# Optimization experiments

Measured on AMD Instinct MI355X. Metric: run time of the kernel, lower is better.

The kernel has to match this reference:

```python
import jax, jax.numpy as jnp
import numpy as np

B, D_IN, N, L, P, C = 512, 784, 2048, 6, 15, 10  # batch, input, width, dag layers, weight pairs, classes


def setup_inputs() -> dict:
    key = jax.random.key(0)
    ks = jax.random.split(key, 10)
    x = jax.random.normal(ks[0], (B, D_IN), jnp.float32)
    w_in = jax.random.normal(ks[1], (N, D_IN), jnp.float32) * 0.1
    b_in = jax.random.normal(ks[2], (N,), jnp.float32) * 0.1
    W = jax.random.normal(ks[3], (P, N, N), jnp.float32) * 0.1
    # binary 0/1 float masks standing in for DAG connectivity masks
    M = jax.random.bernoulli(ks[4], 0.5, (P, N, N)).astype(jnp.float32)
    b = jax.random.normal(ks[5], (L - 1, N), jnp.float32) * 0.1
    w_out1 = jax.random.normal(ks[6], (C, N), jnp.float32) * 0.1
    b_out1 = jax.random.normal(ks[7], (C,), jnp.float32) * 0.1
    w_out2 = jax.random.normal(ks[8], (C, N), jnp.float32) * 0.1
    b_out2 = jax.random.normal(ks[9], (C,), jnp.float32) * 0.1
    return {"x": x, "w_in": w_in, "b_in": b_in, "W": W, "M": M, "b": b,
            "w_out1": w_out1, "b_out1": b_out1, "w_out2": w_out2, "b_out2": b_out2}


def reference(x, w_in, b_in, W, M, b, w_out1, b_out1, w_out2, b_out2):
    # input layer
    acts = [jax.nn.relu(x @ w_in.T + b_in)]  # [B, N]
    idx = 0
    for i in range(1, L):  # DAG layer i has predecessors 0..i-1
        Wm = W[idx:idx + i] * M[idx:idx + i]          # [i, N, N] masked weights
        stacked = jnp.stack(acts)                      # [i, B, N]
        # sum over predecessors of inp @ Wm.T; bias added once per predecessor
        out = jnp.einsum('jbn,jmn->bm', stacked, Wm) + i * b[i - 1]
        acts.append(jax.nn.relu(out))
        idx += i
    return acts[-1] @ w_out1.T + b_out1 + acts[-2] @ w_out2.T + b_out2
```

## Files before the change

### kernel.cpp

```cpp
#include <hip/hip_runtime.h>

typedef __bf16 bf16;
typedef __attribute__((ext_vector_type(8))) __bf16 bf16x8;
typedef __attribute__((ext_vector_type(4))) __bf16 bf16x4;
typedef __attribute__((ext_vector_type(4))) float floatx4;

#define B_SZ 512
#define N_SZ 2048
#define DIN  784
#define DINP 800
#define ACT_LD 12288

__device__ __forceinline__ void load_lds16(const bf16* g, bf16* l) {
    __builtin_amdgcn_global_load_lds(
        (const __attribute__((address_space(1))) void*)g,
        (__attribute__((address_space(3))) void*)l, 16, 0, 0);
}

__global__ __launch_bounds__(256)
void prep_kernel(const float* __restrict__ x, const float* __restrict__ w_in,
                 bf16* __restrict__ xb, bf16* __restrict__ w_inb)
{
    int g = blockIdx.x * 256 + threadIdx.x;
    const int GPR = DINP / 4;
    const float* src; bf16* dst; int row, c;
    if (g < B_SZ * GPR) {
        row = g / GPR; c = g - row * GPR;
        src = x + (size_t)row * DIN;  dst = xb + (size_t)row * DINP;
    } else {
        int h = g - B_SZ * GPR;
        row = h / GPR; c = h - row * GPR;
        src = w_in + (size_t)row * DIN;  dst = w_inb + (size_t)row * DINP;
    }
    int k = c * 4;
    floatx4 v = (floatx4){0.f, 0.f, 0.f, 0.f};
    if (k < DIN) v = *(const floatx4*)(src + k);
    bf16x4 o;
    o[0] = (bf16)v[0]; o[1] = (bf16)v[1]; o[2] = (bf16)v[2]; o[3] = (bf16)v[3];
    *(bf16x4*)(dst + k) = o;
}

__global__ __launch_bounds__(256, 2)
void gemm_kernel(const bf16* __restrict__ A, int lda,
                 const bf16* __restrict__ Bm, int ldb,
                 float* __restrict__ partial,
                 int chunkK, int Ktot)
{
    __shared__ bf16 As[128 * 32];
    __shared__ bf16 Bs[128 * 32];

    const int t    = threadIdx.x;
    const int lane = t & 63, wave = t >> 6;
    const int wm   = (wave & 1) * 64, wn = (wave >> 1) * 64;
    const int l15  = lane & 15, quad = lane >> 4;
    const int n0   = blockIdx.x * 128, m0 = blockIdx.y * 128;
    const int s    = blockIdx.z;
    const int kb   = s * chunkK;
    const int ke   = (kb + chunkK < Ktot) ? (kb + chunkK) : Ktot;

    const int rA = wave * 16 + (lane >> 2);
    const int cA = (lane & 3) * 8;
    const bf16* pA0 = A  + (size_t)(m0 + rA) * lda + cA + kb;
    const bf16* pA1 = pA0 + (size_t)64 * lda;
    const bf16* pB0 = Bm + (size_t)(n0 + rA) * ldb + cA + kb;
    const bf16* pB1 = pB0 + (size_t)64 * ldb;
    bf16* dA0 = &As[wave * 512];  bf16* dA1 = &As[(wave + 4) * 512];
    bf16* dB0 = &Bs[wave * 512];  bf16* dB1 = &Bs[(wave + 4) * 512];

    floatx4 acc[4][4];
#pragma unroll
    for (int a = 0; a < 4; a++)
#pragma unroll
        for (int b = 0; b < 4; b++) acc[a][b] = (floatx4){0.f, 0.f, 0.f, 0.f};

    for (int k0 = kb; k0 < ke; k0 += 32) {
        __syncthreads();
        load_lds16(pA0, dA0);  load_lds16(pA1, dA1);
        load_lds16(pB0, dB0);  load_lds16(pB1, dB1);
        pA0 += 32; pA1 += 32; pB0 += 32; pB1 += 32;
        __syncthreads();

        bf16x8 af[4], bfr[4];
#pragma unroll
        for (int a = 0; a < 4; a++)
            af[a] = *(const bf16x8*)(&As[(wm + a * 16 + l15) * 32 + quad * 8]);
#pragma unroll
        for (int b = 0; b < 4; b++)
            bfr[b] = *(const bf16x8*)(&Bs[(wn + b * 16 + l15) * 32 + quad * 8]);
#pragma unroll
        for (int a = 0; a < 4; a++)
#pragma unroll
            for (int b = 0; b < 4; b++)
                acc[a][b] = __builtin_amdgcn_mfma_f32_16x16x32_bf16(af[a], bfr[b], acc[a][b], 0, 0, 0);
    }

    float* outp = partial + (size_t)s * (B_SZ * N_SZ);
#pragma unroll
    for (int a = 0; a < 4; a++)
#pragma unroll
        for (int b = 0; b < 4; b++)
#pragma unroll
            for (int r = 0; r < 4; r++) {
                int row = m0 + wm + a * 16 + quad * 4 + r;
                int col = n0 + wn + b * 16 + l15;
                outp[(size_t)row * N_SZ + col] = acc[a][b][r];
            }
}

__global__ __launch_bounds__(256, 2)
void dag_gemm_kernel(const bf16* __restrict__ A,
                     const float* __restrict__ Wl, const float* __restrict__ Ml,
                     float* __restrict__ partial,
                     int chunkK, int Ktot)
{
    __shared__ bf16 As[256 * 32];
    __shared__ bf16 Bs[64 * 32];

    const int t    = threadIdx.x;
    const int lane = t & 63, wave = t >> 6;
    const int l15  = lane & 15, quad = lane >> 4;
    const int n0   = blockIdx.x * 64, m0 = blockIdx.y * 256;
    const int s    = blockIdx.z;
    const int kb   = s * chunkK;
    const int ke   = kb + chunkK;

    const int ar = wave * 16 + (lane >> 2);
    const int ac = (lane & 3) * 8;
    const bf16* pA0 = A + (size_t)(m0 +   0 + ar) * ACT_LD + kb + ac;
    const bf16* pA1 = A + (size_t)(m0 +  64 + ar) * ACT_LD + kb + ac;
    const bf16* pA2 = A + (size_t)(m0 + 128 + ar) * ACT_LD + kb + ac;
    const bf16* pA3 = A + (size_t)(m0 + 192 + ar) * ACT_LD + kb + ac;
    bf16* dA0 = &As[(  0 + wave * 16) * 32];
    bf16* dA1 = &As[( 64 + wave * 16) * 32];
    bf16* dA2 = &As[(128 + wave * 16) * 32];
    bf16* dA3 = &As[(192 + wave * 16) * 32];

    const int br = t >> 2, bc = (t & 3) * 8;
    const size_t wrow = (size_t)(n0 + br) << 11;

    floatx4 acc[4][4];
#pragma unroll
    for (int a = 0; a < 4; a++)
#pragma unroll
        for (int b = 0; b < 4; b++) acc[a][b] = (floatx4){0.f, 0.f, 0.f, 0.f};

    floatx4 wr0, wr1, mr0, mr1;
    {
        int jj = kb >> 11, kk = kb & 2047;
        size_t o = ((size_t)jj << 22) + wrow + kk + bc;
        wr0 = *(const floatx4*)(Wl + o);  wr1 = *(const floatx4*)(Wl + o + 4);
        mr0 = *(const floatx4*)(Ml + o);  mr1 = *(const floatx4*)(Ml + o + 4);
    }

    for (int k0 = kb; k0 < ke; k0 += 32) {
        __syncthreads();
        load_lds16(pA0, dA0);  load_lds16(pA1, dA1);
        load_lds16(pA2, dA2);  load_lds16(pA3, dA3);
        pA0 += 32; pA1 += 32; pA2 += 32; pA3 += 32;

        bf16x8 o8;
        o8[0] = (bf16)(wr0[0] * mr0[0]); o8[1] = (bf16)(wr0[1] * mr0[1]);
        o8[2] = (bf16)(wr0[2] * mr0[2]); o8[3] = (bf16)(wr0[3] * mr0[3]);
        o8[4] = (bf16)(wr1[0] * mr1[0]); o8[5] = (bf16)(wr1[1] * mr1[1]);
        o8[6] = (bf16)(wr1[2] * mr1[2]); o8[7] = (bf16)(wr1[3] * mr1[3]);
        *(bf16x8*)(&Bs[br * 32 + bc]) = o8;

        if (k0 + 32 < ke) {
            int kn = k0 + 32;
            int jj = kn >> 11, kk = kn & 2047;
            size_t o = ((size_t)jj << 22) + wrow + kk + bc;
            wr0 = *(const floatx4*)(Wl + o);  wr1 = *(const floatx4*)(Wl + o + 4);
            mr0 = *(const floatx4*)(Ml + o);  mr1 = *(const floatx4*)(Ml + o + 4);
        }
        __syncthreads();

        bf16x8 af[4], bfr[4];
#pragma unroll
        for (int a = 0; a < 4; a++)
            af[a] = *(const bf16x8*)(&As[(wave * 64 + a * 16 + l15) * 32 + quad * 8]);
#pragma unroll
        for (int b = 0; b < 4; b++)
            bfr[b] = *(const bf16x8*)(&Bs[(b * 16 + l15) * 32 + quad * 8]);
#pragma unroll
        for (int a = 0; a < 4; a++)
#pragma unroll
            for (int b = 0; b < 4; b++)
                acc[a][b] = __builtin_amdgcn_mfma_f32_16x16x32_bf16(af[a], bfr[b], acc[a][b], 0, 0, 0);
    }

    float* outp = partial + (size_t)s * (B_SZ * N_SZ);
#pragma unroll
    for (int a = 0; a < 4; a++)
#pragma unroll
        for (int b = 0; b < 4; b++)
#pragma unroll
            for (int r = 0; r < 4; r++) {
                int row = m0 + wave * 64 + a * 16 + quad * 4 + r;
                int col = n0 + b * 16 + l15;
                outp[(size_t)row * N_SZ + col] = acc[a][b][r];
            }
}

__global__ __launch_bounds__(256)
void epilogue_kernel(const float* __restrict__ partial, int S,
                     const float* __restrict__ bias, float bscale,
                     bf16* __restrict__ actdst)
{
    int g = blockIdx.x * 256 + threadIdx.x;
    size_t off = (size_t)g * 4;
    int b = (int)(off >> 11);
    int n = (int)(off & (N_SZ - 1));
    floatx4 v = *(const floatx4*)(partial + off);
    for (int s2 = 1; s2 < S; s2++)
        v += *(const floatx4*)(partial + (size_t)s2 * (B_SZ * N_SZ) + off);
    floatx4 bv = *(const floatx4*)(bias + n);
    bf16x4 o;
#pragma unroll
    for (int j = 0; j < 4; j++) {
        float xv = v[j] + bscale * bv[j];
        xv = xv > 0.f ? xv : 0.f;
        o[j] = (bf16)xv;
    }
    *(bf16x4*)(actdst + (size_t)b * ACT_LD + n) = o;
}

__global__ __launch_bounds__(64)
void out_kernel(const bf16* __restrict__ act4, const bf16* __restrict__ act5,
                const float* __restrict__ w1, const float* __restrict__ b1,
                const float* __restrict__ w2, const float* __restrict__ b2,
                float* __restrict__ out)
{
    int b = blockIdx.x, lane = threadIdx.x;
    float a5[32], a4[32];
#pragma unroll
    for (int rep = 0; rep < 4; rep++) {
        bf16x8 v5 = *(const bf16x8*)(act5 + (size_t)b * ACT_LD + rep * 512 + lane * 8);
        bf16x8 v4 = *(const bf16x8*)(act4 + (size_t)b * ACT_LD + rep * 512 + lane * 8);
#pragma unroll
        for (int j = 0; j < 8; j++) {
            a5[rep * 8 + j] = (float)v5[j];
            a4[rep * 8 + j] = (float)v4[j];
        }
    }
    for (int c = 0; c < 10; c++) {
        float d = 0.f;
#pragma unroll
        for (int rep = 0; rep < 4; rep++) {
            floatx4 wa = *(const floatx4*)(w1 + (size_t)c * N_SZ + rep * 512 + lane * 8);
            floatx4 wb = *(const floatx4*)(w1 + (size_t)c * N_SZ + rep * 512 + lane * 8 + 4);
            floatx4 va = *(const floatx4*)(w2 + (size_t)c * N_SZ + rep * 512 + lane * 8);
            floatx4 vb = *(const floatx4*)(w2 + (size_t)c * N_SZ + rep * 512 + lane * 8 + 4);
#pragma unroll
            for (int j = 0; j < 4; j++) {
                d += a5[rep * 8 + j] * wa[j] + a4[rep * 8 + j] * va[j];
                d += a5[rep * 8 + 4 + j] * wb[j] + a4[rep * 8 + 4 + j] * vb[j];
            }
        }
        for (int off = 32; off > 0; off >>= 1) d += __shfl_down(d, off);
        if (lane == 0) out[b * 10 + c] = d + b1[c] + b2[c];
    }
}

extern "C" void kernel_launch(void* const* d_in, const int* in_sizes, int n_in,
                              void* d_out, int out_size, void* d_ws, size_t ws_size,
                              hipStream_t stream)
{
    const float* x    = (const float*)d_in[0];
    const float* w_in = (const float*)d_in[1];
    const float* b_in = (const float*)d_in[2];
    const float* W    = (const float*)d_in[3];
    const float* M    = (const float*)d_in[4];
    const float* bL   = (const float*)d_in[5];
    const float* w1   = (const float*)d_in[6];
    const float* b1   = (const float*)d_in[7];
    const float* w2   = (const float*)d_in[8];
    const float* b2   = (const float*)d_in[9];
    float* out = (float*)d_out;

    char* ws = (char*)d_ws;
    bf16*  xb      = (bf16*)ws;
    bf16*  w_inb   = (bf16*)(ws + 819200);
    bf16*  actsT   = (bf16*)(ws + 4096000);
    float* partial = (float*)(ws + 16678912);

    prep_kernel<<<2000, 256, 0, stream>>>(x, w_in, xb, w_inb);

    gemm_kernel<<<dim3(16, 4, 4), 256, 0, stream>>>(
        xb, DINP, w_inb, DINP, partial, 224, DINP);
    epilogue_kernel<<<1024, 256, 0, stream>>>(partial, 4, b_in, 1.0f, actsT);

    for (int i = 1; i < 6; i++) {
        int idx = i * (i - 1) / 2;
        const float* Wl = W + ((size_t)idx << 22);
        const float* Ml = M + ((size_t)idx << 22);
        dag_gemm_kernel<<<dim3(32, 2, 8), 256, 0, stream>>>(
            actsT, Wl, Ml, partial, 256 * i, 2048 * i);
        epilogue_kernel<<<1024, 256, 0, stream>>>(
            partial, 8, bL + (size_t)(i - 1) * N_SZ, (float)i,
            actsT + (size_t)i * N_SZ);
    }

    out_kernel<<<512, 64, 0, stream>>>(
        actsT + (size_t)4 * N_SZ, actsT + (size_t)5 * N_SZ,
        w1, b1, w2, b2, out);
}
```

Baseline: 714.2 us.

## Double-buffer LDS in DAG GEMM with register-staged prefetch

Replaces the direct global-to-LDS loads of the activation tile with register-staged loads and double-buffers both the A and B shared-memory tiles. This removes one of the two barriers per K step, and the next tile's global loads are issued before the MFMA work on the current tile so they overlap. In exchange it doubles LDS use, adds register pressure from holding A fragments, and adds explicit LDS stores for A. The unused Ktot parameter is dropped.

```diff
diff --git a/kernel.cpp b/kernel.cpp
--- a/kernel.cpp
+++ b/kernel.cpp
@@ -111,30 +111,20 @@
 void dag_gemm_kernel(const bf16* __restrict__ A,
                      const float* __restrict__ Wl, const float* __restrict__ Ml,
                      float* __restrict__ partial,
-                     int chunkK, int Ktot)
-{
-    __shared__ bf16 As[256 * 32];
-    __shared__ bf16 Bs[64 * 32];
+                     int chunkK)
+{
+    __shared__ bf16 As[2][256 * 32];
+    __shared__ bf16 Bs[2][64 * 32];
 
     const int t    = threadIdx.x;
     const int lane = t & 63, wave = t >> 6;
     const int l15  = lane & 15, quad = lane >> 4;
     const int n0   = blockIdx.x * 64, m0 = blockIdx.y * 256;
-    const int s    = blockIdx.z;
-    const int kb   = s * chunkK;
+    const int kb   = blockIdx.z * chunkK;
     const int ke   = kb + chunkK;
 
     const int ar = wave * 16 + (lane >> 2);
     const int ac = (lane & 3) * 8;
-    const bf16* pA0 = A + (size_t)(m0 +   0 + ar) * ACT_LD + kb + ac;
-    const bf16* pA1 = A + (size_t)(m0 +  64 + ar) * ACT_LD + kb + ac;
-    const bf16* pA2 = A + (size_t)(m0 + 128 + ar) * ACT_LD + kb + ac;
-    const bf16* pA3 = A + (size_t)(m0 + 192 + ar) * ACT_LD + kb + ac;
-    bf16* dA0 = &As[(  0 + wave * 16) * 32];
-    bf16* dA1 = &As[( 64 + wave * 16) * 32];
-    bf16* dA2 = &As[(128 + wave * 16) * 32];
-    bf16* dA3 = &As[(192 + wave * 16) * 32];
-
     const int br = t >> 2, bc = (t & 3) * 8;
     const size_t wrow = (size_t)(n0 + br) << 11;
 
@@ -144,51 +134,55 @@
 #pragma unroll
         for (int b = 0; b < 4; b++) acc[a][b] = (floatx4){0.f, 0.f, 0.f, 0.f};
 
-    floatx4 wr0, wr1, mr0, mr1;
-    {
-        int jj = kb >> 11, kk = kb & 2047;
+    bf16x8 a0, a1, a2, a3;
+    floatx4 wv0, wv1, mv0, mv1;
+
+    auto load_regs = [&](int k) {
+        const bf16* ap = A + (size_t)(m0 + ar) * ACT_LD + k + ac;
+        a0 = *(const bf16x8*)(ap);
+        a1 = *(const bf16x8*)(ap + (size_t)64  * ACT_LD);
+        a2 = *(const bf16x8*)(ap + (size_t)128 * ACT_LD);
+        a3 = *(const bf16x8*)(ap + (size_t)192 * ACT_LD);
+        int jj = k >> 11, kk = k & 2047;
         size_t o = ((size_t)jj << 22) + wrow + kk + bc;
-        wr0 = *(const floatx4*)(Wl + o);  wr1 = *(const floatx4*)(Wl + o + 4);
-        mr0 = *(const floatx4*)(Ml + o);  mr1 = *(const floatx4*)(Ml + o + 4);
-    }
-
-    for (int k0 = kb; k0 < ke; k0 += 32) {
+        wv0 = *(const floatx4*)(Wl + o);  wv1 = *(const floatx4*)(Wl + o + 4);
+        mv0 = *(const floatx4*)(Ml + o);  mv1 = *(const floatx4*)(Ml + o + 4);
+    };
+
+    auto do_step = [&](int buf, int knext, bool pref) {
+        bf16x8 o8;
+        o8[0] = (bf16)(wv0[0] * mv0[0]); o8[1] = (bf16)(wv0[1] * mv0[1]);
+        o8[2] = (bf16)(wv0[2] * mv0[2]); o8[3] = (bf16)(wv0[3] * mv0[3]);
+        o8[4] = (bf16)(wv1[0] * mv1[0]); o8[5] = (bf16)(wv1[1] * mv1[1]);
+        o8[6] = (bf16)(wv1[2] * mv1[2]); o8[7] = (bf16)(wv1[3] * mv1[3]);
+        *(bf16x8*)(&Bs[buf][br * 32 + bc]) = o8;
+        *(bf16x8*)(&As[buf][(ar +   0) * 32 + ac]) = a0;
+        *(bf16x8*)(&As[buf][(ar +  64) * 32 + ac]) = a1;
+        *(bf16x8*)(&As[buf][(ar + 128) * 32 + ac]) = a2;
+        *(bf16x8*)(&As[buf][(ar + 192) * 32 + ac]) = a3;
+        if (pref) load_regs(knext);
         __syncthreads();
-        load_lds16(pA0, dA0);  load_lds16(pA1, dA1);
-        load_lds16(pA2, dA2);  load_lds16(pA3, dA3);
-        pA0 += 32; pA1 += 32; pA2 += 32; pA3 += 32;
-
-        bf16x8 o8;
-        o8[0] = (bf16)(wr0[0] * mr0[0]); o8[1] = (bf16)(wr0[1] * mr0[1]);
-        o8[2] = (bf16)(wr0[2] * mr0[2]); o8[3] = (bf16)(wr0[3] * mr0[3]);
-        o8[4] = (bf16)(wr1[0] * mr1[0]); o8[5] = (bf16)(wr1[1] * mr1[1]);
-        o8[6] = (bf16)(wr1[2] * mr1[2]); o8[7] = (bf16)(wr1[3] * mr1[3]);
-        *(bf16x8*)(&Bs[br * 32 + bc]) = o8;
-
-        if (k0 + 32 < ke) {
-            int kn = k0 + 32;
-            int jj = kn >> 11, kk = kn & 2047;
-            size_t o = ((size_t)jj << 22) + wrow + kk + bc;
-            wr0 = *(const floatx4*)(Wl + o);  wr1 = *(const floatx4*)(Wl + o + 4);
-            mr0 = *(const floatx4*)(Ml + o);  mr1 = *(const floatx4*)(Ml + o + 4);
-        }
-        __syncthreads();
-
         bf16x8 af[4], bfr[4];
 #pragma unroll
         for (int a = 0; a < 4; a++)
-            af[a] = *(const bf16x8*)(&As[(wave * 64 + a * 16 + l15) * 32 + quad * 8]);
+            af[a] = *(const bf16x8*)(&As[buf][(wave * 64 + a * 16 + l15) * 32 + quad * 8]);
 #pragma unroll
         for (int b = 0; b < 4; b++)
-            bfr[b] = *(const bf16x8*)(&Bs[(b * 16 + l15) * 32 + quad * 8]);
+            bfr[b] = *(const bf16x8*)(&Bs[buf][(b * 16 + l15) * 32 + quad * 8]);
 #pragma unroll
         for (int a = 0; a < 4; a++)
 #pragma unroll
             for (int b = 0; b < 4; b++)
                 acc[a][b] = __builtin_amdgcn_mfma_f32_16x16x32_bf16(af[a], bfr[b], acc[a][b], 0, 0, 0);
-    }
-
-    float* outp = partial + (size_t)s * (B_SZ * N_SZ);
+    };
+
+    load_regs(kb);
+    for (int k0 = kb; k0 < ke; k0 += 64) {
+        do_step(0, k0 + 32, true);
+        do_step(1, k0 + 64, (k0 + 64) < ke);
+    }
+
+    float* outp = partial + (size_t)blockIdx.z * (B_SZ * N_SZ);
 #pragma unroll
     for (int a = 0; a < 4; a++)
 #pragma unroll
@@ -294,7 +288,7 @@
         const float* Wl = W + ((size_t)idx << 22);
         const float* Ml = M + ((size_t)idx << 22);
         dag_gemm_kernel<<<dim3(32, 2, 8), 256, 0, stream>>>(
-            actsT, Wl, Ml, partial, 256 * i, 2048 * i);
+            actsT, Wl, Ml, partial, 256 * i);
         epilogue_kernel<<<1024, 256, 0, stream>>>(
             partial, 8, bL + (size_t)(i - 1) * N_SZ, (float)i,
             actsT + (size_t)i * N_SZ);
```

Result: faster. 691.5 us (-3.2%).
